# Optimization experiments

Measured on AMD Instinct MI355X. Metric: run time of the kernel, lower is better.

Reference implementation:

```python
import jax, jax.numpy as jnp
import numpy as np

B, L, D_MODEL, H = 2, 1920, 512, 8
DEPTH = D_MODEL // H
MAX_REL = 1921


def skew(t):
    """Huang et al. 2018 skew: pad, reshape, slice. t: (..., L, L)."""
    Lq, Lk = t.shape[-2], t.shape[-1]
    padded = jnp.pad(t, [(0, 0)] * (t.ndim - 1) + [(1, 0)])  # (..., Lq, Lk+1)
    s = padded.reshape(-1, Lk + 1, Lq)[:, 1:]                 # drop first row
    return s.reshape(t.shape)


def setup_inputs() -> dict:
    key = jax.random.key(0)
    ks = jax.random.split(key, 12)
    w = lambda k, shp: (jax.random.normal(k, shp, jnp.float32) * 0.02)
    inp = {
        "q": jax.random.normal(ks[0], (B, L, D_MODEL), jnp.float32),
        "k": jax.random.normal(ks[1], (B, L, D_MODEL), jnp.float32),
        "v": jax.random.normal(ks[2], (B, L, D_MODEL), jnp.float32),
        "mask": jnp.triu(jnp.ones((L, L), jnp.float32), k=1)[None, None],  # causal look-ahead
        "Wq": w(ks[3], (D_MODEL, D_MODEL)), "bq": jnp.zeros((D_MODEL,), jnp.float32),
        "Wk": w(ks[4], (D_MODEL, D_MODEL)), "bk": jnp.zeros((D_MODEL,), jnp.float32),
        "Wv": w(ks[5], (D_MODEL, D_MODEL)), "bv": jnp.zeros((D_MODEL,), jnp.float32),
        "E": w(ks[6], (MAX_REL, D_MODEL)),
        "Wo": w(ks[7], (D_MODEL, D_MODEL)), "bo": jnp.zeros((D_MODEL,), jnp.float32),
    }
    return inp


def reference(q, k, v, mask, Wq, bq, Wk, bk, Wv, bv, E, Wo, bo):
    Lk = k.shape[-2]
    qp = q @ Wq + bq
    kp = k @ Wk + bk
    vp = v @ Wv + bv
    # required relative embeddings (max_len >= seq_len branch): rightmost Lk rows
    e = E[MAX_REL - Lk:]                                   # (Lk, d_model)
    # split heads
    qh = qp.reshape(B, -1, H, DEPTH).transpose(0, 2, 1, 3)  # (B,H,Lq,depth)
    kh = kp.reshape(B, Lk, H, DEPTH).transpose(0, 2, 1, 3)
    vh = vp.reshape(B, Lk, H, DEPTH).transpose(0, 2, 1, 3)
    eh = e.reshape(Lk, H, DEPTH).transpose(1, 0, 2)         # (H,Lk,depth)
    QKt = jnp.einsum('bhqd,bhkd->bhqk', qh, kh)
    Srel = skew(jnp.einsum('bhqd,hkd->bhqk', qh, eh))
    logits = (QKt + Srel) / jnp.sqrt(jnp.float32(DEPTH))
    logits = logits + mask * (-1e9)
    attn = jax.nn.softmax(logits, axis=-1)                  # (B,H,Lq,Lk)
    out = jnp.einsum('bhqk,bhkd->bhqd', attn, vh)
    out = out.transpose(0, 2, 1, 3).reshape(B, -1, D_MODEL)
    out = out @ Wo + bo
    return out, attn
```

## Files before the change

### kernel.cpp

```cpp
#include <hip/hip_runtime.h>

typedef unsigned short u16;
typedef short s16x8 __attribute__((ext_vector_type(8)));
typedef float f32x4 __attribute__((ext_vector_type(4)));

#define MFMA_BF16(a, b, c) __builtin_amdgcn_mfma_f32_16x16x32_bf16((a), (b), (c), 0, 0, 0)

#define L_SEQ 1920
#define DM    512
#define NH    8
#define CH    6
#define NCHB  90

#define GLL16(gp, lp) __builtin_amdgcn_global_load_lds(                       \
    (const __attribute__((address_space(1))) void*)(gp),                      \
    (__attribute__((address_space(3))) void*)(lp), 16, 0, 0)

__device__ __forceinline__ u16 f2b(float f) {
  union { float f; unsigned u; } a; a.f = f;
  unsigned u = a.u;
  u += 0x7fffu + ((u >> 16) & 1u);
  return (u16)(u >> 16);
}
__device__ __forceinline__ float b2f(u16 h) {
  union { unsigned u; float f; } a; a.u = ((unsigned)h) << 16;
  return a.f;
}
__device__ __forceinline__ float rsum16(float x) {
  x += __shfl_xor(x, 1);
  x += __shfl_xor(x, 2);
  x += __shfl_xor(x, 4);
  x += __shfl_xor(x, 8);
  return x;
}

__global__ __launch_bounds__(256) void cvt_kernel(
    const float* __restrict__ q, const float* __restrict__ k,
    const float* __restrict__ v, const float* __restrict__ E,
    u16* __restrict__ qc, u16* __restrict__ kc,
    u16* __restrict__ vc, u16* __restrict__ Ec,
    const float* __restrict__ Wq, const float* __restrict__ Wk,
    const float* __restrict__ Wv, const float* __restrict__ Wo,
    u16* __restrict__ Wqt, u16* __restrict__ Wkt,
    u16* __restrict__ Wvt, u16* __restrict__ Wot) {
  __shared__ u16 T[64][72];
  if (blockIdx.y == 4) {
    const int bx = blockIdx.x;
    if (bx >= 256) return;
    const float* W; u16* Wt;
    const int z = bx >> 6;
    if (z == 0)      { W = Wq; Wt = Wqt; }
    else if (z == 1) { W = Wk; Wt = Wkt; }
    else if (z == 2) { W = Wv; Wt = Wvt; }
    else             { W = Wo; Wt = Wot; }
    const int rem = bx & 63;
    const int k0 = (rem >> 3) * 64, n0 = (rem & 7) * 64;
    const int r = threadIdx.x >> 2, c = (threadIdx.x & 3) * 16;
#pragma unroll
    for (int i = 0; i < 4; ++i) {
      float4 f = *(const float4*)(W + (size_t)(k0 + r) * 512 + n0 + c + i * 4);
      ushort4 u; u.x = f2b(f.x); u.y = f2b(f.y); u.z = f2b(f.z); u.w = f2b(f.w);
      *(ushort4*)&T[r][c + i * 4] = u;
    }
    __syncthreads();
    u16 tmp[16];
#pragma unroll
    for (int i = 0; i < 16; ++i) tmp[i] = T[c + i][r];
    u16* dst = Wt + (size_t)(n0 + r) * 512 + k0 + c;
    *(uint4*)dst       = *(uint4*)tmp;
    *(uint4*)(dst + 8) = *(uint4*)(tmp + 8);
    return;
  }
  const float* src; u16* dst; int n;
  if (blockIdx.y == 0)      { src = q; dst = qc; n = 1966080; }
  else if (blockIdx.y == 1) { src = k; dst = kc; n = 1966080; }
  else if (blockIdx.y == 2) { src = v; dst = vc; n = 1966080; }
  else                      { src = E; dst = Ec; n = 983552; }
  const int i = (blockIdx.x * 256 + threadIdx.x) * 8;
  if (i < n) {
    float4 a = *(const float4*)(src + i);
    float4 b = *(const float4*)(src + i + 4);
    ushort4 ua; ua.x = f2b(a.x); ua.y = f2b(a.y); ua.z = f2b(a.z); ua.w = f2b(a.w);
    ushort4 ub; ub.x = f2b(b.x); ub.y = f2b(b.y); ub.z = f2b(b.z); ub.w = f2b(b.w);
    *(ushort4*)(dst + i)     = ua;
    *(ushort4*)(dst + i + 4) = ub;
  }
}

__global__ __launch_bounds__(256) void vtrans_kernel(const u16* __restrict__ vp,
                                                     u16* __restrict__ vt) {
  const int bh = blockIdx.y, k0 = blockIdx.x * 64;
  const int b = bh >> 3, h = bh & 7;
  __shared__ u16 T[64][72];
  const int r = threadIdx.x >> 2, c = (threadIdx.x & 3) * 16;
  const u16* src = vp + (size_t)(b * L_SEQ + k0 + r) * DM + h * 64 + c;
  *(uint4*)&T[r][c]     = *(const uint4*)src;
  *(uint4*)&T[r][c + 8] = *(const uint4*)(src + 8);
  __syncthreads();
  u16 tmp[16];
#pragma unroll
  for (int i = 0; i < 16; ++i) tmp[i] = T[c + i][r];
  u16* dst = vt + (size_t)bh * 64 * L_SEQ + (size_t)r * L_SEQ + k0 + c;
  *(uint4*)dst       = *(uint4*)tmp;
  *(uint4*)(dst + 8) = *(uint4*)(tmp + 8);
}

template<bool OBF>
__device__ __forceinline__ void gemm512_body(const u16* Ap, const u16* Wt,
                                             const float* bias, void* Cp) {
  __shared__ u16 As[128 * 32];
  __shared__ u16 Bs[128 * 32];
  const int tid  = threadIdx.x;
  const int wv   = tid >> 6, lane = tid & 63, quad = lane >> 4, l16 = lane & 15;
  const int wr   = wv >> 1, wc = wv & 1;
  const int row0 = blockIdx.x * 128, n0 = blockIdx.y * 128;

  const int srow = tid >> 2, scol = (tid & 3) * 8;
  const u16* sA = Ap + (size_t)(row0 + srow) * 512 + scol;
  const u16* sB = Wt + (size_t)(n0  + srow) * 512 + scol;

  f32x4 acc[4][4];
#pragma unroll
  for (int i = 0; i < 4; ++i)
#pragma unroll
    for (int j = 0; j < 4; ++j) acc[i][j] = {0.f, 0.f, 0.f, 0.f};

  for (int kt = 0; kt < 16; ++kt) {
    const int k0 = kt * 32;
    GLL16(sA + k0,             &As[wv * 512]);
    GLL16(sA + k0 + 64 * 512,  &As[2048 + wv * 512]);
    GLL16(sB + k0,             &Bs[wv * 512]);
    GLL16(sB + k0 + 64 * 512,  &Bs[2048 + wv * 512]);
    __syncthreads();
    s16x8 af[4], bfr[4];
#pragma unroll
    for (int i = 0; i < 4; ++i)
      af[i]  = *(const s16x8*)&As[(wr * 64 + i * 16 + l16) * 32 + quad * 8];
#pragma unroll
    for (int i = 0; i < 4; ++i)
      bfr[i] = *(const s16x8*)&Bs[(wc * 64 + i * 16 + l16) * 32 + quad * 8];
#pragma unroll
    for (int am = 0; am < 4; ++am)
#pragma unroll
      for (int bn = 0; bn < 4; ++bn)
        acc[am][bn] = MFMA_BF16(af[am], bfr[bn], acc[am][bn]);
    __syncthreads();
  }

#pragma unroll
  for (int am = 0; am < 4; ++am)
#pragma unroll
    for (int bn = 0; bn < 4; ++bn)
#pragma unroll
      for (int r = 0; r < 4; ++r) {
        const int row = row0 + wr * 64 + am * 16 + quad * 4 + r;
        const int col = n0 + wc * 64 + bn * 16 + l16;
        float v = acc[am][bn][r] + bias[col];
        if constexpr (OBF) ((u16*)Cp)[(size_t)row * 512 + col] = f2b(v);
        else               ((float*)Cp)[(size_t)row * 512 + col] = v;
      }
}

__global__ __launch_bounds__(256) void proj3_kernel(
    const u16* __restrict__ qc, const u16* __restrict__ kc, const u16* __restrict__ vc,
    const u16* __restrict__ Wqt, const u16* __restrict__ Wkt, const u16* __restrict__ Wvt,
    const float* __restrict__ bq, const float* __restrict__ bk, const float* __restrict__ bv,
    u16* __restrict__ qp, u16* __restrict__ kp, u16* __restrict__ vp) {
  const u16* A; const u16* W; const float* bias; u16* C;
  if (blockIdx.z == 0)      { A = qc; W = Wqt; bias = bq; C = qp; }
  else if (blockIdx.z == 1) { A = kc; W = Wkt; bias = bk; C = kp; }
  else                      { A = vc; W = Wvt; bias = bv; C = vp; }
  gemm512_body<true>(A, W, bias, C);
}

__global__ __launch_bounds__(256) void outproj_kernel(
    const u16* __restrict__ A, const u16* __restrict__ Wot,
    const float* __restrict__ bo, float* __restrict__ out) {
  gemm512_body<false>(A, Wot, bo, out);
}

__global__ __launch_bounds__(256) void flash_kernel(
    const u16* __restrict__ qp, const u16* __restrict__ kp, const u16* __restrict__ vt,
    const u16* __restrict__ Ec, u16* __restrict__ phat,
    float* __restrict__ opart, float* __restrict__ spart) {
  __shared__ u16 PW[4][16][136];

  const int wg  = blockIdx.x;
  const int swz = (wg & 7) * 180 + (wg >> 3);
  const int cid0 = swz % NCHB;
  const int bh   = swz / NCHB;
  const int h = bh & 7, b = bh >> 3;

  const int tid = threadIdx.x, wv = tid >> 6, lane = tid & 63;
  const int quad = lane >> 4, l16 = lane & 15;
  const int j0 = 48 - wv * 16;

  int qt = 0, c = cid0;
  for (;;) { const int n = (qt + CH) / CH; if (c < n) break; c -= n; ++qt; }
  const int kts = c * CH, kte = min(qt, kts + CH - 1);
  const int q0 = qt * 64;
  const size_t gcid = (size_t)bh * NCHB + cid0;

  const u16* qb = qp + (size_t)b * L_SEQ * DM + h * 64;
  const u16* kb = kp + (size_t)b * L_SEQ * DM + h * 64;
  const u16* vtb = vt + (size_t)bh * 64 * L_SEQ;
  const u16* Eb = Ec + h * 64;
  u16* pb = phat + ((size_t)bh * L_SEQ + q0) * L_SEQ;

  s16x8 qf[2];
  {
    const u16* src = qb + (size_t)(q0 + wv * 16 + l16) * DM + quad * 8;
    qf[0] = *(const s16x8*)src;
    qf[1] = *(const s16x8*)(src + 32);
  }

  float sr[4] = {0.f, 0.f, 0.f, 0.f};
  f32x4 oacc[4];
#pragma unroll
  for (int i = 0; i < 4; ++i) oacc[i] = {0.f, 0.f, 0.f, 0.f};

  for (int kt = kts; kt <= kte; ++kt) {
    const int k0 = kt * 64;

    f32x4 qa[4], ba[5];
#pragma unroll
    for (int i = 0; i < 4; ++i) qa[i] = {0.f, 0.f, 0.f, 0.f};
#pragma unroll
    for (int i = 0; i < 5; ++i) ba[i] = {0.f, 0.f, 0.f, 0.f};
#pragma unroll
    for (int kk = 0; kk < 2; ++kk) {
      s16x8 kf[4], ef[5];
#pragma unroll
      for (int t = 0; t < 4; ++t)
        kf[t] = *(const s16x8*)(kb + (size_t)(k0 + t * 16 + l16) * DM + kk * 32 + quad * 8);
#pragma unroll
      for (int u = 0; u < 5; ++u) {
        int rg = k0 + (L_SEQ - 64) - q0 + j0 + u * 16 + l16;
        rg = rg < 0 ? 0 : (rg > L_SEQ - 1 ? L_SEQ - 1 : rg);
        ef[u] = *(const s16x8*)(Eb + (size_t)(1 + rg) * DM + kk * 32 + quad * 8);
      }
      __builtin_amdgcn_s_setprio(1);
#pragma unroll
      for (int t = 0; t < 4; ++t) qa[t] = MFMA_BF16(qf[kk], kf[t], qa[t]);
#pragma unroll
      for (int u = 0; u < 5; ++u) ba[u] = MFMA_BF16(qf[kk], ef[u], ba[u]);
      __builtin_amdgcn_s_setprio(0);
    }

#pragma unroll
    for (int u = 0; u < 5; ++u)
#pragma unroll
      for (int r = 0; r < 4; ++r)
        PW[wv][quad * 4 + r][u * 16 + l16] = f2b(ba[u][r]);

    u16 pb16[4][4];
#pragma unroll
    for (int r = 0; r < 4; ++r) {
      const int lr = quad * 4 + r;
      const int qi = wv * 16 + lr;
      float ssum = 0.f;
#pragma unroll
      for (int t = 0; t < 4; ++t) {
        const float srel = b2f(PW[wv][lr][15 - lr + 16 * t + l16]);
        const float v = (qa[t][r] + srel) * 0.125f;
        const float p = ((k0 + t * 16 + l16) <= (q0 + qi)) ? __expf(v) : 0.f;
        ssum += p;
        pb16[r][t] = f2b(p);
      }
      sr[r] += rsum16(ssum);
    }
#pragma unroll
    for (int t = 0; t < 4; ++t)
#pragma unroll
      for (int r = 0; r < 4; ++r)
        PW[wv][quad * 4 + r][t * 16 + l16] = pb16[r][t];

#pragma unroll
    for (int kk = 0; kk < 2; ++kk) {
      s16x8 pa = *(const s16x8*)&PW[wv][l16][kk * 32 + quad * 8];
      __builtin_amdgcn_s_setprio(1);
#pragma unroll
      for (int db = 0; db < 4; ++db) {
        s16x8 vf = *(const s16x8*)(vtb + (size_t)(db * 16 + l16) * L_SEQ + k0 + kk * 32 + quad * 8);
        oacc[db] = MFMA_BF16(pa, vf, oacc[db]);
      }
      __builtin_amdgcn_s_setprio(0);
    }

    {
      const int prow = lane >> 3, pcol = (lane & 7) * 8;
      u16* d0 = pb + (size_t)(wv * 16 + prow) * L_SEQ + k0 + pcol;
      u16* d1 = pb + (size_t)(wv * 16 + 8 + prow) * L_SEQ + k0 + pcol;
      *(uint4*)d0 = *(const uint4*)&PW[wv][prow][pcol];
      *(uint4*)d1 = *(const uint4*)&PW[wv][8 + prow][pcol];
    }
  }

  float* op = opart + gcid * 4096;
#pragma unroll
  for (int db = 0; db < 4; ++db)
#pragma unroll
    for (int r = 0; r < 4; ++r)
      op[(size_t)(wv * 16 + quad * 4 + r) * 64 + db * 16 + l16] = oacc[db][r];
  if (l16 == 0) {
#pragma unroll
    for (int r = 0; r < 4; ++r)
      spart[gcid * 64 + wv * 16 + quad * 4 + r] = sr[r];
  }
}

__global__ __launch_bounds__(256) void merge_kernel(
    const float* __restrict__ opart, const float* __restrict__ spart,
    u16* __restrict__ oc, float* __restrict__ sfin) {
  const int qt = blockIdx.x, bh = blockIdx.y;
  const int b = bh >> 3, h = bh & 7;
  int pre = 0;
  for (int q2 = 0; q2 < qt; ++q2) pre += (q2 + CH) / CH;
  const int nc = (qt + CH) / CH;
  const size_t gc0 = (size_t)bh * NCHB + pre;

  const int qi = threadIdx.x >> 2, ds = (threadIdx.x & 3) * 16;
  float s = 0.f;
  float4 o[4] = {{0,0,0,0},{0,0,0,0},{0,0,0,0},{0,0,0,0}};
  for (int ci = 0; ci < nc; ++ci) {
    s += spart[(gc0 + ci) * 64 + qi];
    const float* op = opart + (gc0 + ci) * 4096 + (size_t)qi * 64 + ds;
#pragma unroll
    for (int i = 0; i < 4; ++i) {
      const float4 a = *(const float4*)(op + i * 4);
      o[i].x += a.x; o[i].y += a.y; o[i].z += a.z; o[i].w += a.w;
    }
  }
  const float inv = 1.0f / s;
  u16* dst = oc + (size_t)(b * L_SEQ + qt * 64 + qi) * DM + h * 64 + ds;
#pragma unroll
  for (int i = 0; i < 4; ++i) {
    ushort4 u;
    u.x = f2b(o[i].x * inv); u.y = f2b(o[i].y * inv);
    u.z = f2b(o[i].z * inv); u.w = f2b(o[i].w * inv);
    *(ushort4*)(dst + i * 4) = u;
  }
  if ((threadIdx.x & 3) == 0) sfin[(size_t)bh * L_SEQ + qt * 64 + qi] = s;
}

__global__ __launch_bounds__(256) void fixup_kernel(
    const u16* __restrict__ phat, const float* __restrict__ sfin,
    float* __restrict__ attn) {
  const int bh = blockIdx.y;
  const int r  = blockIdx.x * 8 + (threadIdx.x >> 5);
  const int lc = threadIdx.x & 31;
  const int nlow = ((r >> 6) + 1) * 64;
  const size_t rowidx = (size_t)bh * L_SEQ + r;
  const u16* prow = phat + rowidx * L_SEQ;
  float* arow = attn + rowidx * L_SEQ;
  const float fac = 1.0f / sfin[rowidx];
#pragma unroll
  for (int j = 0; j < 15; ++j) {
    const int col = (lc + j * 32) * 4;
    float4 o;
    if (col < nlow) {
      uint2 u = *(const uint2*)(prow + col);
      o.x = b2f((u16)(u.x & 0xffff)) * fac;  o.y = b2f((u16)(u.x >> 16)) * fac;
      o.z = b2f((u16)(u.y & 0xffff)) * fac;  o.w = b2f((u16)(u.y >> 16)) * fac;
    } else {
      o = {0.f, 0.f, 0.f, 0.f};
    }
    *(float4*)(arow + col) = o;
  }
}

extern "C" void kernel_launch(void* const* d_in, const int* in_sizes, int n_in,
                              void* d_out, int out_size, void* d_ws, size_t ws_size,
                              hipStream_t stream) {
  const float* q  = (const float*)d_in[0];
  const float* k  = (const float*)d_in[1];
  const float* v  = (const float*)d_in[2];
  const float* Wq = (const float*)d_in[4];
  const float* bq = (const float*)d_in[5];
  const float* Wk = (const float*)d_in[6];
  const float* bk = (const float*)d_in[7];
  const float* Wv = (const float*)d_in[8];
  const float* bv = (const float*)d_in[9];
  const float* E  = (const float*)d_in[10];
  const float* Wo = (const float*)d_in[11];
  const float* bo = (const float*)d_in[12];

  float* out  = (float*)d_out;
  float* attn = out + (size_t)3840 * 512;

  u16* qc  = (u16*)d_ws;
  u16* kc  = qc + 1966080;
  u16* vc  = kc + 1966080;
  u16* Wqt = vc + 1966080;
  u16* Wkt = Wqt + 262144;
  u16* Wvt = Wkt + 262144;
  u16* Wot = Wvt + 262144;
  u16* Ec  = Wot + 262144;
  u16* qp  = Ec + 983552;
  u16* kp  = qp + 1966080;
  u16* vp  = kp + 1966080;
  u16* vt  = vp + 1966080;
  u16* oc  = vt + 1966080;
  u16* phat = oc + 1966080;
  float* opart = (float*)(phat + 58982400);
  float* spart = opart + (size_t)1440 * 4096;
  float* sfin  = spart + 1440 * 64;

  cvt_kernel<<<dim3(960, 5), 256, 0, stream>>>(q, k, v, E, qc, kc, vc, Ec,
                                               Wq, Wk, Wv, Wo, Wqt, Wkt, Wvt, Wot);
  proj3_kernel<<<dim3(30, 4, 3), 256, 0, stream>>>(qc, kc, vc, Wqt, Wkt, Wvt,
                                                   bq, bk, bv, qp, kp, vp);
  vtrans_kernel<<<dim3(30, 16), 256, 0, stream>>>(vp, vt);
  flash_kernel<<<dim3(1440), 256, 0, stream>>>(qp, kp, vt, Ec, phat, opart, spart);
  merge_kernel<<<dim3(30, 16), 256, 0, stream>>>(opart, spart, oc, sfin);
  fixup_kernel<<<dim3(240, 16), 256, 0, stream>>>(phat, sfin, attn);
  outproj_kernel<<<dim3(30, 4), 256, 0, stream>>>(oc, Wot, bo, out);
}
```

Before: 468.4 us.

## Stage K, V and E tiles in LDS with register prefetch in flash kernel

Each key tile's K, transposed V and relative-embedding E rows are now loaded cooperatively by the whole workgroup into shared memory. The next tile is prefetched into registers while the current one is computed. Previously every wave loaded its own fragments straight from global memory, so four waves fetched the same K/V data redundantly. The change adds about 35 KB of LDS and two barriers per tile, and removes the s_setprio hints, which may reduce occupancy.

```diff
diff --git a/kernel.cpp b/kernel.cpp
--- a/kernel.cpp
+++ b/kernel.cpp
@@ -183,6 +183,9 @@
     const u16* __restrict__ qp, const u16* __restrict__ kp, const u16* __restrict__ vt,
     const u16* __restrict__ Ec, u16* __restrict__ phat,
     float* __restrict__ opart, float* __restrict__ spart) {
+  __shared__ u16 Ks[64][72];
+  __shared__ u16 Vs[64][72];
+  __shared__ u16 Es[128][72];
   __shared__ u16 PW[4][16][136];
 
   const int wg  = blockIdx.x;
@@ -214,13 +217,48 @@
     qf[1] = *(const s16x8*)(src + 32);
   }
 
-  float sr[4] = {0.f, 0.f, 0.f, 0.f};
+  const int sr = tid >> 2, sc = (tid & 3) * 16;
+  const int ej = tid >> 1, ec = (tid & 1) * 32;
+
+  uint4 rK0, rK1, rV0, rV1, rE0, rE1, rE2, rE3;
+  {
+    const int k0 = kts * 64;
+    const u16* ksrc = kb + (size_t)(k0 + sr) * DM + sc;
+    rK0 = *(const uint4*)ksrc; rK1 = *(const uint4*)(ksrc + 8);
+    const u16* vsrc = vtb + (size_t)sr * L_SEQ + k0 + sc;
+    rV0 = *(const uint4*)vsrc; rV1 = *(const uint4*)(vsrc + 8);
+    int rg = k0 + (L_SEQ - 64) - q0 + ej;
+    rg = rg < 0 ? 0 : (rg > L_SEQ - 1 ? L_SEQ - 1 : rg);
+    const u16* esrc = Eb + (size_t)(1 + rg) * DM + ec;
+    rE0 = *(const uint4*)esrc;        rE1 = *(const uint4*)(esrc + 8);
+    rE2 = *(const uint4*)(esrc + 16); rE3 = *(const uint4*)(esrc + 24);
+  }
+
+  float sr4[4] = {0.f, 0.f, 0.f, 0.f};
   f32x4 oacc[4];
 #pragma unroll
   for (int i = 0; i < 4; ++i) oacc[i] = {0.f, 0.f, 0.f, 0.f};
 
   for (int kt = kts; kt <= kte; ++kt) {
     const int k0 = kt * 64;
+    *(uint4*)&Ks[sr][sc]     = rK0;  *(uint4*)&Ks[sr][sc + 8]  = rK1;
+    *(uint4*)&Vs[sr][sc]     = rV0;  *(uint4*)&Vs[sr][sc + 8]  = rV1;
+    *(uint4*)&Es[ej][ec]     = rE0;  *(uint4*)&Es[ej][ec + 8]  = rE1;
+    *(uint4*)&Es[ej][ec + 16] = rE2; *(uint4*)&Es[ej][ec + 24] = rE3;
+    __syncthreads();
+
+    if (kt < kte) {
+      const int k1 = k0 + 64;
+      const u16* ksrc = kb + (size_t)(k1 + sr) * DM + sc;
+      rK0 = *(const uint4*)ksrc; rK1 = *(const uint4*)(ksrc + 8);
+      const u16* vsrc = vtb + (size_t)sr * L_SEQ + k1 + sc;
+      rV0 = *(const uint4*)vsrc; rV1 = *(const uint4*)(vsrc + 8);
+      int rg = k1 + (L_SEQ - 64) - q0 + ej;
+      rg = rg < 0 ? 0 : (rg > L_SEQ - 1 ? L_SEQ - 1 : rg);
+      const u16* esrc = Eb + (size_t)(1 + rg) * DM + ec;
+      rE0 = *(const uint4*)esrc;        rE1 = *(const uint4*)(esrc + 8);
+      rE2 = *(const uint4*)(esrc + 16); rE3 = *(const uint4*)(esrc + 24);
+    }
 
     f32x4 qa[4], ba[5];
 #pragma unroll
@@ -229,24 +267,17 @@
     for (int i = 0; i < 5; ++i) ba[i] = {0.f, 0.f, 0.f, 0.f};
 #pragma unroll
     for (int kk = 0; kk < 2; ++kk) {
-      s16x8 kf[4], ef[5];
-#pragma unroll
-      for (int t = 0; t < 4; ++t)
-        kf[t] = *(const s16x8*)(kb + (size_t)(k0 + t * 16 + l16) * DM + kk * 32 + quad * 8);
+#pragma unroll
+      for (int t = 0; t < 4; ++t) {
+        s16x8 kf = *(const s16x8*)&Ks[t * 16 + l16][kk * 32 + quad * 8];
+        qa[t] = MFMA_BF16(qf[kk], kf, qa[t]);
+      }
 #pragma unroll
       for (int u = 0; u < 5; ++u) {
-        int rg = k0 + (L_SEQ - 64) - q0 + j0 + u * 16 + l16;
-        rg = rg < 0 ? 0 : (rg > L_SEQ - 1 ? L_SEQ - 1 : rg);
-        ef[u] = *(const s16x8*)(Eb + (size_t)(1 + rg) * DM + kk * 32 + quad * 8);
+        s16x8 ef = *(const s16x8*)&Es[j0 + u * 16 + l16][kk * 32 + quad * 8];
+        ba[u] = MFMA_BF16(qf[kk], ef, ba[u]);
       }
-      __builtin_amdgcn_s_setprio(1);
-#pragma unroll
-      for (int t = 0; t < 4; ++t) qa[t] = MFMA_BF16(qf[kk], kf[t], qa[t]);
-#pragma unroll
-      for (int u = 0; u < 5; ++u) ba[u] = MFMA_BF16(qf[kk], ef[u], ba[u]);
-      __builtin_amdgcn_s_setprio(0);
-    }
-
+    }
 #pragma unroll
     for (int u = 0; u < 5; ++u)
 #pragma unroll
@@ -267,7 +298,7 @@
         ssum += p;
         pb16[r][t] = f2b(p);
       }
-      sr[r] += rsum16(ssum);
+      sr4[r] += rsum16(ssum);
     }
 #pragma unroll
     for (int t = 0; t < 4; ++t)
@@ -278,13 +309,11 @@
 #pragma unroll
     for (int kk = 0; kk < 2; ++kk) {
       s16x8 pa = *(const s16x8*)&PW[wv][l16][kk * 32 + quad * 8];
-      __builtin_amdgcn_s_setprio(1);
 #pragma unroll
       for (int db = 0; db < 4; ++db) {
-        s16x8 vf = *(const s16x8*)(vtb + (size_t)(db * 16 + l16) * L_SEQ + k0 + kk * 32 + quad * 8);
+        s16x8 vf = *(const s16x8*)&Vs[db * 16 + l16][kk * 32 + quad * 8];
         oacc[db] = MFMA_BF16(pa, vf, oacc[db]);
       }
-      __builtin_amdgcn_s_setprio(0);
     }
 
     {
@@ -294,6 +323,7 @@
       *(uint4*)d0 = *(const uint4*)&PW[wv][prow][pcol];
       *(uint4*)d1 = *(const uint4*)&PW[wv][8 + prow][pcol];
     }
+    __syncthreads();
   }
 
   float* op = opart + gcid * 4096;
@@ -305,7 +335,7 @@
   if (l16 == 0) {
 #pragma unroll
     for (int r = 0; r < 4; ++r)
-      spart[gcid * 64 + wv * 16 + quad * 4 + r] = sr[r];
+      spart[gcid * 64 + wv * 16 + quad * 4 + r] = sr4[r];
   }
 }
 
```

Result: faster. 418.1 us (-10.7%).
